# Optimization experiments

Measured on AMD Instinct MI355X. Metric: run time of the kernel, lower is better.

The kernel has to match this reference:

```python
import jax, jax.numpy as jnp
import numpy as np

N = 100000          # number of nodes (src == dst in this sampled graph)
DEG = 8             # uniform sampled fan-in (max_num_neighbors)
E = N * DEG         # number of edges
IN_C = 128
HEADS = 4
OUT_C = 32
NEG_SLOPE = 0.2


def setup_inputs() -> dict:
    key = jax.random.key(0)
    k1, k2, k3, k4, k5 = jax.random.split(key, 5)
    x = jax.random.normal(k1, (N, IN_C), dtype=jnp.float32)
    csr_row_ptr = jnp.arange(N + 1, dtype=jnp.int64) * DEG
    csr_col_ind = jax.random.randint(k2, (E,), 0, N, dtype=jnp.int64)
    # learned params (xavier-normal-ish scaling)
    lin_w = jax.random.normal(k3, (IN_C, HEADS * OUT_C), dtype=jnp.float32) * np.sqrt(2.0 / (IN_C + HEADS * OUT_C))
    att = jax.random.normal(k4, (2 * HEADS * OUT_C,), dtype=jnp.float32) * np.sqrt(2.0 / (1 + OUT_C))
    bias = jnp.zeros((HEADS * OUT_C,), dtype=jnp.float32)
    return {"x": x, "csr_row_ptr": csr_row_ptr, "csr_col_ind": csr_col_ind,
            "max_num_neighbors": DEG, "lin_w": lin_w, "att": att, "bias": bias}


def reference(x, csr_row_ptr, csr_col_ind, max_num_neighbors, lin_w, att, bias):
    n = x.shape[0]
    e = csr_col_ind.shape[0]
    hc = HEADS * OUT_C
    # linear projection: [N, H, C]
    xp = (x @ lin_w).reshape(n, HEADS, OUT_C)
    att_src = att[:hc].reshape(HEADS, OUT_C)
    att_dst = att[hc:].reshape(HEADS, OUT_C)
    # per-node attention logits per head: [N, H]
    a_src = jnp.einsum('nhc,hc->nh', xp, att_src)
    a_dst = jnp.einsum('nhc,hc->nh', xp, att_dst)
    # expand CSR row_ptr into per-edge destination ids: [E]
    dst = jnp.searchsorted(csr_row_ptr, jnp.arange(e, dtype=csr_row_ptr.dtype), side='right') - 1
    src = csr_col_ind
    # edge scores + per-destination softmax over incoming edges
    logits = jax.nn.leaky_relu(a_src[src] + a_dst[dst], NEG_SLOPE)  # [E, H]
    m = jax.ops.segment_max(logits, dst, num_segments=n)            # [N, H]
    ex = jnp.exp(logits - m[dst])
    denom = jax.ops.segment_sum(ex, dst, num_segments=n)            # [N, H]
    alpha = ex / denom[dst]                                         # [E, H]
    # weighted aggregation of neighbor features: [N, H, C]
    out = jax.ops.segment_sum(alpha[:, :, None] * xp[src], dst, num_segments=n)
    out = out.reshape(n, hc) + bias  # concat=True
    return out
```

## Files before the change

### kernel.cpp

```cpp
#include <hip/hip_runtime.h>
#include <stdint.h>

#define HEADS 4
#define NEG_SLOPE 0.2f
#define MB 64

typedef _Float16 f16;
typedef f16 f16x8 __attribute__((ext_vector_type(8)));
typedef f16 f16x4 __attribute__((ext_vector_type(4)));
typedef float f32x4 __attribute__((ext_vector_type(4)));

#define SWZ(row, kb) (((row) << 8) + ((kb) ^ (((row) & 7) << 4)))

__global__ __launch_bounds__(256) void wt_kernel(const float* __restrict__ w,
                                                 f16* __restrict__ wt) {
    __shared__ f16 tl[16][136];
    const int b = blockIdx.x, t = threadIdx.x;
    for (int i = t; i < 2048; i += 256) {
        int k = i >> 4, nl = i & 15;
        tl[nl][k] = (f16)w[k * 128 + b * 16 + nl];
    }
    __syncthreads();
    {
        int nl = t >> 4, kc = t & 15;
        f16x8 v = *(const f16x8*)&tl[nl][kc * 8];
        *(f16x8*)(wt + (b * 16 + nl) * 128 + kc * 8) = v;
    }
}

__global__ __launch_bounds__(256) void gat_proj_mfma(
    const float* __restrict__ x, const f16* __restrict__ wt,
    const float* __restrict__ att, f16* __restrict__ xp,
    float* __restrict__ a_src, float* __restrict__ a_dst, int n) {
    __shared__ unsigned char lds[49152];
    __shared__ float att_l[256];
    const int t = threadIdx.x;
    const int node0 = blockIdx.x * MB;
    const int lane = t & 63;
    const int wv = t >> 6;

    att_l[t] = att[t];

    for (int i = t; i < 2048; i += 256) {
        int row = i >> 4, kc = i & 15;
        uint4 v = *(const uint4*)(wt + row * 128 + kc * 8);
        *(uint4*)(lds + SWZ(row, kc * 16)) = v;
    }
    for (int i = t; i < 1024; i += 256) {
        int row = i >> 4, kc = i & 15;
        int grow = node0 + row;
        float4 a = make_float4(0.f, 0.f, 0.f, 0.f), b = a;
        if (grow < n) {
            const float4* p = (const float4*)(x + (size_t)grow * 128 + kc * 8);
            a = p[0];
            b = p[1];
        }
        f16x8 hv;
        hv[0] = (f16)a.x; hv[1] = (f16)a.y; hv[2] = (f16)a.z; hv[3] = (f16)a.w;
        hv[4] = (f16)b.x; hv[5] = (f16)b.y; hv[6] = (f16)b.z; hv[7] = (f16)b.w;
        *(f16x8*)(lds + 32768 + SWZ(row, kc * 16)) = hv;
    }
    __syncthreads();

    f32x4 acc[8];
#pragma unroll
    for (int nf = 0; nf < 8; nf++) acc[nf] = (f32x4){0.f, 0.f, 0.f, 0.f};

#pragma unroll
    for (int kt = 0; kt < 4; kt++) {
        const int kb = kt * 64 + (lane >> 4) * 16;
        int arow = wv * 16 + (lane & 15);
        f16x8 afr = *(const f16x8*)(lds + 32768 + SWZ(arow, kb));
#pragma unroll
        for (int nf = 0; nf < 8; nf++) {
            int wrow = nf * 16 + (lane & 15);
            f16x8 bfr = *(const f16x8*)(lds + SWZ(wrow, kb));
            acc[nf] = __builtin_amdgcn_mfma_f32_16x16x32_f16(afr, bfr, acc[nf], 0, 0, 0);
        }
    }

    __syncthreads();
#pragma unroll
    for (int r = 0; r < 4; r++) {
        int row = wv * 16 + (lane >> 4) * 4 + r;
#pragma unroll
        for (int nf = 0; nf < 8; nf++) {
            int col = nf * 16 + (lane & 15);
            *(f16*)(lds + 32768 + SWZ(row, col * 2)) = (f16)acc[nf][r];
        }
    }
    __syncthreads();

    {
        int row = t >> 2, h = t & 3;
        int grow = node0 + row;
        if (grow < n) {
            float s = 0.f, d = 0.f;
#pragma unroll
            for (int cc = 0; cc < 4; cc++) {
                f16x8 v = *(const f16x8*)(lds + 32768 + SWZ(row, h * 64 + cc * 16));
#pragma unroll
                for (int j = 0; j < 8; j++) {
                    float xv = (float)v[j];
                    int c = cc * 8 + j;
                    s = fmaf(xv, att_l[h * 32 + c], s);
                    d = fmaf(xv, att_l[128 + h * 32 + c], d);
                }
            }
            a_src[(size_t)grow * HEADS + h] = s;
            a_dst[(size_t)grow * HEADS + h] = d;
        }
    }
    for (int i = t; i < 1024; i += 256) {
        int row = i >> 4, kc = i & 15;
        int grow = node0 + row;
        if (grow < n)
            *(uint4*)(xp + (size_t)grow * 128 + kc * 8) =
                *(const uint4*)(lds + 32768 + SWZ(row, kc * 16));
    }
}

__global__ __launch_bounds__(256) void gat_aggr_kernel(
    const f16* __restrict__ xp, const float* __restrict__ a_src,
    const float* __restrict__ a_dst, const int* __restrict__ row_ptr,
    const int* __restrict__ col_ind, const float* __restrict__ bias,
    float* __restrict__ out, int n) {
    const int lane = threadIdx.x & 63;
    const int p = lane >> 5, l = lane & 31;
    const int nb = (blockIdx.x * 4 + (threadIdx.x >> 6)) * 2;
    if (nb >= n) return;

    int rp = 0;
    if (lane < 3) {
        int idx = nb + lane;
        if (idx > n) idx = n;
        rp = row_ptr[idx];
    }
    int rs0 = __shfl(rp, 0, 64), rs1 = __shfl(rp, 1, 64), re1 = __shfl(rp, 2, 64);
    int deg0 = rs1 - rs0, deg1 = re1 - rs1;
    if (deg0 > 8) deg0 = 8;
    if (deg1 > 8) deg1 = 8;
    if (nb + 1 >= n) deg1 = 0;

    int ci = 0;
    if (lane < 16) {
        int j = lane >> 3, e = lane & 7;
        int rs = j ? rs1 : rs0;
        int dg = j ? deg1 : deg0;
        if (e < dg) ci = col_ind[rs + e];
    }

    f16x4 pv[8];
#pragma unroll
    for (int k = 0; k < 8; k++) {
        int j = k >> 2, e = 2 * (k & 3) + p;
        int s = __shfl(ci, j * 8 + e, 64);
        pv[k] = *(const f16x4*)(xp + (size_t)s * 128 + l * 4);
    }

    const int ea = (l >> 2) & 7, ha = l & 3;
    const int dg = p ? deg1 : deg0;
    int sa = __shfl(ci, p * 8 + ea, 64);
    float v = -1e30f;
    if (ea < dg) {
        float z = a_src[(size_t)sa * HEADS + ha] + a_dst[(size_t)(nb + p) * HEADS + ha];
        v = (z >= 0.f) ? z : NEG_SLOPE * z;
    }
    float m = v;
    m = fmaxf(m, __shfl_xor(m, 4, 64));
    m = fmaxf(m, __shfl_xor(m, 8, 64));
    m = fmaxf(m, __shfl_xor(m, 16, 64));
    float ex = (ea < dg) ? __expf(v - m) : 0.f;
    float ss = ex;
    ss += __shfl_xor(ss, 4, 64);
    ss += __shfl_xor(ss, 8, 64);
    ss += __shfl_xor(ss, 16, 64);
    float alpha = ex * ((ss > 0.f) ? (1.f / ss) : 0.f);

    const int h = l >> 3;
    float acc[2][4] = {{0.f, 0.f, 0.f, 0.f}, {0.f, 0.f, 0.f, 0.f}};
#pragma unroll
    for (int k = 0; k < 4; k++) {
        int e = 2 * k + p;
#pragma unroll
        for (int j = 0; j < 2; j++) {
            float a = __shfl(alpha, j * 32 + e * 4 + h, 64);
            f16x4 pvv = pv[j * 4 + k];
            acc[j][0] = fmaf(a, (float)pvv[0], acc[j][0]);
            acc[j][1] = fmaf(a, (float)pvv[1], acc[j][1]);
            acc[j][2] = fmaf(a, (float)pvv[2], acc[j][2]);
            acc[j][3] = fmaf(a, (float)pvv[3], acc[j][3]);
        }
    }
#pragma unroll
    for (int j = 0; j < 2; j++)
#pragma unroll
        for (int c = 0; c < 4; c++)
            acc[j][c] += __shfl_xor(acc[j][c], 32, 64);

    if (nb + p < n) {
        float4 b4 = ((const float4*)bias)[l];
        float4 o = make_float4(acc[p][0] + b4.x, acc[p][1] + b4.y,
                               acc[p][2] + b4.z, acc[p][3] + b4.w);
        *(float4*)(out + (size_t)(nb + p) * 128 + l * 4) = o;
    }
}

extern "C" void kernel_launch(void* const* d_in, const int* in_sizes, int n_in,
                              void* d_out, int out_size, void* d_ws, size_t ws_size,
                              hipStream_t stream) {
    const float* x = (const float*)d_in[0];
    const int* row_ptr = (const int*)d_in[1];
    const int* col_ind = (const int*)d_in[2];
    const float* lin_w = (const float*)d_in[4];
    const float* att = (const float*)d_in[5];
    const float* bias = (const float*)d_in[6];
    float* out = (float*)d_out;
    const int n = in_sizes[0] / 128;

    f16* xp = (f16*)d_ws;
    float* a_src = (float*)((char*)d_ws + (size_t)n * 128 * 2);
    float* a_dst = a_src + (size_t)n * HEADS;
    f16* wt = (f16*)(a_dst + (size_t)n * HEADS);

    hipLaunchKernelGGL(wt_kernel, dim3(8), dim3(256), 0, stream, lin_w, wt);
    hipLaunchKernelGGL(gat_proj_mfma, dim3((n + MB - 1) / MB), dim3(256), 0, stream,
                       x, wt, att, xp, a_src, a_dst, n);
    hipLaunchKernelGGL(gat_aggr_kernel, dim3((n + 7) / 8), dim3(256), 0, stream,
                       xp, a_src, a_dst, row_ptr, col_ind, bias, out, n);
}
```

Before: 71.32 us.

## Load x fragments directly into registers and process four nodes per wave in aggregation

Result: faster. 69.42 us (-2.7%).

```diff
diff --git a/kernel.cpp b/kernel.cpp
--- a/kernel.cpp
+++ b/kernel.cpp
@@ -9,6 +9,7 @@
 typedef f16 f16x8 __attribute__((ext_vector_type(8)));
 typedef f16 f16x4 __attribute__((ext_vector_type(4)));
 typedef float f32x4 __attribute__((ext_vector_type(4)));
+typedef unsigned int u32x4 __attribute__((ext_vector_type(4)));
 
 #define SWZ(row, kb) (((row) << 8) + ((kb) ^ (((row) & 7) << 4)))
 
@@ -32,7 +33,7 @@
     const float* __restrict__ x, const f16* __restrict__ wt,
     const float* __restrict__ att, f16* __restrict__ xp,
     float* __restrict__ a_src, float* __restrict__ a_dst, int n) {
-    __shared__ unsigned char lds[49152];
+    __shared__ unsigned char lds[32768];
     __shared__ float att_l[256];
     const int t = threadIdx.x;
     const int node0 = blockIdx.x * MB;
@@ -41,25 +42,28 @@
 
     att_l[t] = att[t];
 
+    const int arow = node0 + wv * 16 + (lane & 15);
+    const bool rowok = arow < n;
+    const float* xr = x + (size_t)arow * 128 + (lane >> 4) * 8;
+    f16x8 afr[4];
+#pragma unroll
+    for (int kt = 0; kt < 4; kt++) {
+        float4 a = make_float4(0.f, 0.f, 0.f, 0.f), b = a;
+        if (rowok) {
+            a = *(const float4*)(xr + kt * 32);
+            b = *(const float4*)(xr + kt * 32 + 4);
+        }
+        f16x8 hv;
+        hv[0] = (f16)a.x; hv[1] = (f16)a.y; hv[2] = (f16)a.z; hv[3] = (f16)a.w;
+        hv[4] = (f16)b.x; hv[5] = (f16)b.y; hv[6] = (f16)b.z; hv[7] = (f16)b.w;
+        afr[kt] = hv;
+    }
+
     for (int i = t; i < 2048; i += 256) {
         int row = i >> 4, kc = i & 15;
         uint4 v = *(const uint4*)(wt + row * 128 + kc * 8);
         *(uint4*)(lds + SWZ(row, kc * 16)) = v;
     }
-    for (int i = t; i < 1024; i += 256) {
-        int row = i >> 4, kc = i & 15;
-        int grow = node0 + row;
-        float4 a = make_float4(0.f, 0.f, 0.f, 0.f), b = a;
-        if (grow < n) {
-            const float4* p = (const float4*)(x + (size_t)grow * 128 + kc * 8);
-            a = p[0];
-            b = p[1];
-        }
-        f16x8 hv;
-        hv[0] = (f16)a.x; hv[1] = (f16)a.y; hv[2] = (f16)a.z; hv[3] = (f16)a.w;
-        hv[4] = (f16)b.x; hv[5] = (f16)b.y; hv[6] = (f16)b.z; hv[7] = (f16)b.w;
-        *(f16x8*)(lds + 32768 + SWZ(row, kc * 16)) = hv;
-    }
     __syncthreads();
 
     f32x4 acc[8];
@@ -69,13 +73,10 @@
 #pragma unroll
     for (int kt = 0; kt < 4; kt++) {
         const int kb = kt * 64 + (lane >> 4) * 16;
-        int arow = wv * 16 + (lane & 15);
-        f16x8 afr = *(const f16x8*)(lds + 32768 + SWZ(arow, kb));
 #pragma unroll
         for (int nf = 0; nf < 8; nf++) {
-            int wrow = nf * 16 + (lane & 15);
-            f16x8 bfr = *(const f16x8*)(lds + SWZ(wrow, kb));
-            acc[nf] = __builtin_amdgcn_mfma_f32_16x16x32_f16(afr, bfr, acc[nf], 0, 0, 0);
+            f16x8 bfr = *(const f16x8*)(lds + SWZ(nf * 16 + (lane & 15), kb));
+            acc[nf] = __builtin_amdgcn_mfma_f32_16x16x32_f16(afr[kt], bfr, acc[nf], 0, 0, 0);
         }
     }
 
@@ -86,7 +87,7 @@
 #pragma unroll
         for (int nf = 0; nf < 8; nf++) {
             int col = nf * 16 + (lane & 15);
-            *(f16*)(lds + 32768 + SWZ(row, col * 2)) = (f16)acc[nf][r];
+            *(f16*)(lds + SWZ(row, col * 2)) = (f16)acc[nf][r];
         }
     }
     __syncthreads();
@@ -98,7 +99,7 @@
             float s = 0.f, d = 0.f;
 #pragma unroll
             for (int cc = 0; cc < 4; cc++) {
-                f16x8 v = *(const f16x8*)(lds + 32768 + SWZ(row, h * 64 + cc * 16));
+                f16x8 v = *(const f16x8*)(lds + SWZ(row, h * 64 + cc * 16));
 #pragma unroll
                 for (int j = 0; j < 8; j++) {
                     float xv = (float)v[j];
@@ -114,9 +115,10 @@
     for (int i = t; i < 1024; i += 256) {
         int row = i >> 4, kc = i & 15;
         int grow = node0 + row;
-        if (grow < n)
-            *(uint4*)(xp + (size_t)grow * 128 + kc * 8) =
-                *(const uint4*)(lds + 32768 + SWZ(row, kc * 16));
+        if (grow < n) {
+            u32x4 v = *(const u32x4*)(lds + SWZ(row, kc * 16));
+            __builtin_nontemporal_store(v, (u32x4*)(xp + (size_t)grow * 128 + kc * 8));
+        }
     }
 }
 
@@ -124,85 +126,113 @@
     const f16* __restrict__ xp, const float* __restrict__ a_src,
     const float* __restrict__ a_dst, const int* __restrict__ row_ptr,
     const int* __restrict__ col_ind, const float* __restrict__ bias,
-    float* __restrict__ out, int n) {
+    float* __restrict__ out, int n, int e_total) {
     const int lane = threadIdx.x & 63;
     const int p = lane >> 5, l = lane & 31;
-    const int nb = (blockIdx.x * 4 + (threadIdx.x >> 6)) * 2;
+    const int nb = (blockIdx.x * 4 + (threadIdx.x >> 6)) * 4;
     if (nb >= n) return;
 
     int rp = 0;
-    if (lane < 3) {
+    if (lane < 5) {
         int idx = nb + lane;
         if (idx > n) idx = n;
         rp = row_ptr[idx];
     }
-    int rs0 = __shfl(rp, 0, 64), rs1 = __shfl(rp, 1, 64), re1 = __shfl(rp, 2, 64);
-    int deg0 = rs1 - rs0, deg1 = re1 - rs1;
-    if (deg0 > 8) deg0 = 8;
-    if (deg1 > 8) deg1 = 8;
-    if (nb + 1 >= n) deg1 = 0;
-
     int ci = 0;
-    if (lane < 16) {
+    {
+        int si = nb * 8 + lane;
+        if (lane < 32 && si < e_total) ci = col_ind[si];
+    }
+    float4 b4 = ((const float4*)bias)[l];
+
+    int rs0 = __shfl(rp, 0, 64), rs1 = __shfl(rp, 1, 64), rs2 = __shfl(rp, 2, 64);
+    int rs3 = __shfl(rp, 3, 64), rs4 = __shfl(rp, 4, 64);
+    int dg0 = rs1 - rs0, dg1 = rs2 - rs1, dg2 = rs3 - rs2, dg3 = rs4 - rs3;
+    if (dg0 > 8) dg0 = 8;
+    if (dg1 > 8) dg1 = 8;
+    if (dg2 > 8) dg2 = 8;
+    if (dg3 > 8) dg3 = 8;
+    if (nb + 1 >= n) dg1 = 0;
+    if (nb + 2 >= n) dg2 = 0;
+    if (nb + 3 >= n) dg3 = 0;
+    bool ok = (nb + 4 <= n) && (rs0 == nb * 8) && (rs1 == rs0 + 8) &&
+              (rs2 == rs1 + 8) && (rs3 == rs2 + 8) && (rs4 == rs3 + 8);
+    if (!ok) {
         int j = lane >> 3, e = lane & 7;
-        int rs = j ? rs1 : rs0;
-        int dg = j ? deg1 : deg0;
-        if (e < dg) ci = col_ind[rs + e];
-    }
-
-    f16x4 pv[8];
-#pragma unroll
-    for (int k = 0; k < 8; k++) {
+        int rsj = (j == 0) ? rs0 : (j == 1) ? rs1 : (j == 2) ? rs2 : rs3;
+        int dgj = (j == 0) ? dg0 : (j == 1) ? dg1 : (j == 2) ? dg2 : dg3;
+        int v = 0;
+        if (lane < 32 && e < dgj) v = col_ind[rsj + e];
+        ci = v;
+    }
+
+    f16x4 pv[16];
+#pragma unroll
+    for (int k = 0; k < 16; k++) {
         int j = k >> 2, e = 2 * (k & 3) + p;
         int s = __shfl(ci, j * 8 + e, 64);
         pv[k] = *(const f16x4*)(xp + (size_t)s * 128 + l * 4);
     }
 
     const int ea = (l >> 2) & 7, ha = l & 3;
-    const int dg = p ? deg1 : deg0;
-    int sa = __shfl(ci, p * 8 + ea, 64);
-    float v = -1e30f;
-    if (ea < dg) {
-        float z = a_src[(size_t)sa * HEADS + ha] + a_dst[(size_t)(nb + p) * HEADS + ha];
-        v = (z >= 0.f) ? z : NEG_SLOPE * z;
-    }
-    float m = v;
-    m = fmaxf(m, __shfl_xor(m, 4, 64));
-    m = fmaxf(m, __shfl_xor(m, 8, 64));
-    m = fmaxf(m, __shfl_xor(m, 16, 64));
-    float ex = (ea < dg) ? __expf(v - m) : 0.f;
-    float ss = ex;
-    ss += __shfl_xor(ss, 4, 64);
-    ss += __shfl_xor(ss, 8, 64);
-    ss += __shfl_xor(ss, 16, 64);
-    float alpha = ex * ((ss > 0.f) ? (1.f / ss) : 0.f);
+    const int dsel0 = p ? dg1 : dg0;
+    const int dsel1 = p ? dg3 : dg2;
+    int sa0 = __shfl(ci, (0 * 2 + p) * 8 + ea, 64);
+    int sa1 = __shfl(ci, (1 * 2 + p) * 8 + ea, 64);
+    float av0 = (ea < dsel0) ? a_src[(size_t)sa0 * HEADS + ha] : 0.f;
+    float av1 = (ea < dsel1) ? a_src[(size_t)sa1 * HEADS + ha] : 0.f;
+    float dv0 = (nb + p < n) ? a_dst[(size_t)(nb + p) * HEADS + ha] : 0.f;
+    float dv1 = (nb + 2 + p < n) ? a_dst[(size_t)(nb + 2 + p) * HEADS + ha] : 0.f;
+
+    float alpha[2];
+#pragma unroll
+    for (int q = 0; q < 2; q++) {
+        const int dsel = q ? dsel1 : dsel0;
+        float z = (q ? av1 : av0) + (q ? dv1 : dv0);
+        float v = (ea < dsel) ? ((z >= 0.f) ? z : NEG_SLOPE * z) : -1e30f;
+        float m = v;
+        m = fmaxf(m, __shfl_xor(m, 4, 64));
+        m = fmaxf(m, __shfl_xor(m, 8, 64));
+        m = fmaxf(m, __shfl_xor(m, 16, 64));
+        float ex = (ea < dsel) ? __expf(v - m) : 0.f;
+        float ss = ex;
+        ss += __shfl_xor(ss, 4, 64);
+        ss += __shfl_xor(ss, 8, 64);
+        ss += __shfl_xor(ss, 16, 64);
+        alpha[q] = ex * ((ss > 0.f) ? (1.f / ss) : 0.f);
+    }
 
     const int h = l >> 3;
-    float acc[2][4] = {{0.f, 0.f, 0.f, 0.f}, {0.f, 0.f, 0.f, 0.f}};
-#pragma unroll
-    for (int k = 0; k < 4; k++) {
-        int e = 2 * k + p;
-#pragma unroll
-        for (int j = 0; j < 2; j++) {
-            float a = __shfl(alpha, j * 32 + e * 4 + h, 64);
-            f16x4 pvv = pv[j * 4 + k];
-            acc[j][0] = fmaf(a, (float)pvv[0], acc[j][0]);
-            acc[j][1] = fmaf(a, (float)pvv[1], acc[j][1]);
-            acc[j][2] = fmaf(a, (float)pvv[2], acc[j][2]);
-            acc[j][3] = fmaf(a, (float)pvv[3], acc[j][3]);
-        }
-    }
-#pragma unroll
-    for (int j = 0; j < 2; j++)
+    float acc[4][4] = {{0.f, 0.f, 0.f, 0.f}, {0.f, 0.f, 0.f, 0.f},
+                       {0.f, 0.f, 0.f, 0.f}, {0.f, 0.f, 0.f, 0.f}};
+#pragma unroll
+    for (int k = 0; k < 16; k++) {
+        const int j = k >> 2;
+        int e = 2 * (k & 3) + p;
+        float a = __shfl(alpha[j >> 1], (j & 1) * 32 + e * 4 + h, 64);
+        f16x4 pvv = pv[k];
+        acc[j][0] = fmaf(a, (float)pvv[0], acc[j][0]);
+        acc[j][1] = fmaf(a, (float)pvv[1], acc[j][1]);
+        acc[j][2] = fmaf(a, (float)pvv[2], acc[j][2]);
+        acc[j][3] = fmaf(a, (float)pvv[3], acc[j][3]);
+    }
+#pragma unroll
+    for (int j = 0; j < 4; j++)
 #pragma unroll
         for (int c = 0; c < 4; c++)
             acc[j][c] += __shfl_xor(acc[j][c], 32, 64);
 
-    if (nb + p < n) {
-        float4 b4 = ((const float4*)bias)[l];
-        float4 o = make_float4(acc[p][0] + b4.x, acc[p][1] + b4.y,
-                               acc[p][2] + b4.z, acc[p][3] + b4.w);
-        *(float4*)(out + (size_t)(nb + p) * 128 + l * 4) = o;
+#pragma unroll
+    for (int q = 0; q < 2; q++) {
+        int j = 2 * q + p;
+        if (nb + j < n) {
+            f32x4 o;
+            o[0] = (p ? acc[2 * q + 1][0] : acc[2 * q][0]) + b4.x;
+            o[1] = (p ? acc[2 * q + 1][1] : acc[2 * q][1]) + b4.y;
+            o[2] = (p ? acc[2 * q + 1][2] : acc[2 * q][2]) + b4.z;
+            o[3] = (p ? acc[2 * q + 1][3] : acc[2 * q][3]) + b4.w;
+            __builtin_nontemporal_store(o, (f32x4*)(out + (size_t)(nb + j) * 128 + l * 4));
+        }
     }
 }
 
@@ -217,6 +247,7 @@
     const float* bias = (const float*)d_in[6];
     float* out = (float*)d_out;
     const int n = in_sizes[0] / 128;
+    const int e_total = in_sizes[2];
 
     f16* xp = (f16*)d_ws;
     float* a_src = (float*)((char*)d_ws + (size_t)n * 128 * 2);
@@ -226,6 +257,6 @@
     hipLaunchKernelGGL(wt_kernel, dim3(8), dim3(256), 0, stream, lin_w, wt);
     hipLaunchKernelGGL(gat_proj_mfma, dim3((n + MB - 1) / MB), dim3(256), 0, stream,
                        x, wt, att, xp, a_src, a_dst, n);
-    hipLaunchKernelGGL(gat_aggr_kernel, dim3((n + 7) / 8), dim3(256), 0, stream,
-                       xp, a_src, a_dst, row_ptr, col_ind, bias, out, n);
-}
+    hipLaunchKernelGGL(gat_aggr_kernel, dim3((n + 15) / 16), dim3(256), 0, stream,
+                       xp, a_src, a_dst, row_ptr, col_ind, bias, out, n, e_total);
+}
```
